# Kernel tuning notes

Hardware: AMD Instinct MI355X
Metric: run time of the kernel (lower is better)

Reference implementation:

```python
import jax, jax.numpy as jnp
import numpy as np
from functools import partial

N_USERS = 30000
N_ENTITIES = 70000
N = N_USERS + N_ENTITIES
D = 64
N_EDGES = 1_600_000
EPS = 1e-12


def setup_inputs() -> dict:
    key = jax.random.key(0)
    ks = jax.random.split(key, 10)
    s = 1.0 / np.sqrt(D)  # xavier-like scale for weights
    return {
        "user_tab": jax.random.normal(ks[0], (N_USERS, D), jnp.float32) * 0.1,
        "entity_tab": jax.random.normal(ks[1], (N_ENTITIES, D), jnp.float32) * 0.1,
        "A_vals": jax.random.uniform(ks[2], (N_EDGES,), jnp.float32) / 16.0,  # ~row-normalized
        "W1_1": jax.random.normal(ks[3], (D, D), jnp.float32) * s,
        "b1_1": jnp.zeros((D,), jnp.float32),
        "W2_1": jax.random.normal(ks[4], (D, D), jnp.float32) * s,
        "b2_1": jnp.zeros((D,), jnp.float32),
        "W1_2": jax.random.normal(ks[5], (D, 32), jnp.float32) * s,
        "b1_2": jnp.zeros((32,), jnp.float32),
        "W2_2": jax.random.normal(ks[6], (D, 32), jnp.float32) * s,
        "b2_2": jnp.zeros((32,), jnp.float32),
        "A_rows": jax.random.randint(ks[7], (N_EDGES,), 0, N, jnp.int64 if jax.config.jax_enable_x64 else jnp.int32),
        "A_cols": jax.random.randint(ks[8], (N_EDGES,), 0, N, jnp.int64 if jax.config.jax_enable_x64 else jnp.int32),
    }


def _spmm(rows, cols, vals, x):
    # sparse A (COO) @ dense x : gather tail embeddings, scale, scatter-add to rows
    msgs = x[cols] * vals[:, None]            # [E, d]
    return jax.ops.segment_sum(msgs, rows, num_segments=N)


def _l2norm(x):
    n = jnp.sqrt(jnp.sum(x * x, axis=1, keepdims=True))
    return x / jnp.maximum(n, EPS)


def _bi_layer(ego, side, W1, b1, W2, b2):
    sum_e = jax.nn.leaky_relu((ego + side) @ W1 + b1)  # slope 0.01 = torch default
    bi_e = jax.nn.leaky_relu((ego * side) @ W2 + b2)
    return _l2norm(sum_e + bi_e)  # dropout p=0 (eval)


def reference(user_tab, entity_tab, A_vals, W1_1, b1_1, W2_1, b2_1,
              W1_2, b1_2, W2_2, b2_2, A_rows, A_cols):
    ego = jnp.concatenate([user_tab, entity_tab], axis=0)  # [N, 64]
    all_embed = [ego]
    # layer 1: 64 -> 64
    side = _spmm(A_rows, A_cols, A_vals, ego)
    ego = _bi_layer(ego, side, W1_1, b1_1, W2_1, b2_1)
    all_embed.append(ego)
    # layer 2: 64 -> 32
    side = _spmm(A_rows, A_cols, A_vals, ego)
    ego = _bi_layer(ego, side, W1_2, b1_2, W2_2, b2_2)
    all_embed.append(ego)
    return jnp.concatenate(all_embed, axis=1)  # [N, 160]; split [n_users, n_entities] downstream
```

## Files before the change

### kernel.cpp

```cpp
#include <hip/hip_runtime.h>
#include <hip/hip_bf16.h>
#include <string.h>

#define N_USERS 30000
#define N_NODES 100000
#define DIM 64
#define N_EDGES 1600000
#define ROWS_PER_BUCK 256
#define NB ((N_NODES + ROWS_PER_BUCK - 1) / ROWS_PER_BUCK)
#define CHUNK 8192
#define NBLK_B ((N_EDGES + CHUNK - 1) / CHUNK)
#define E_ALLOC 1901464
#define STAGE_CAP 5120

typedef __hip_bfloat16 bf16;
typedef __attribute__((ext_vector_type(8))) short short8;
typedef __attribute__((ext_vector_type(4))) float floatx4;

__device__ __forceinline__ float b2f(bf16 v) { return __bfloat162float(v); }
__device__ __forceinline__ bf16 f2b(float v) { return __float2bfloat16(v); }
__device__ __forceinline__ unsigned short fbits(float v) {
    bf16 b = f2b(v); unsigned short u; memcpy(&u, &b, 2); return u;
}
__device__ __forceinline__ float ubf(unsigned u) {
    return __uint_as_float(u << 16);
}

__device__ __forceinline__ float ld(const void* p, int i, int f32) {
    return f32 ? ((const float*)p)[i] : b2f(((const bf16*)p)[i]);
}
__device__ __forceinline__ void st(void* p, int i, float v, int f32) {
    if (f32) ((float*)p)[i] = v; else ((bf16*)p)[i] = f2b(v);
}

__global__ void k_detect(const void* user, const void* ent, const void* vals,
                         const void* W, int* flags, int* bsize) {
    int t = threadIdx.x;
    for (int i = t; i < NB; i += 64) bsize[i] = 0;
    if (t == 0) {
        const void* ps[4] = { user, ent, vals, W };
        for (int k = 0; k < 4; ++k) {
            const float* f = (const float*)ps[k];
            int ok = 0;
            for (int i = 0; i < 32; ++i) {
                float v = f[i];
                if (v == v && fabsf(v) <= 1e4f) ok++;
            }
            flags[k] = (ok >= 16) ? 1 : 0;
        }
    }
}

__global__ __launch_bounds__(256) void k_hista(const int* __restrict__ rows,
                                               int* __restrict__ cnt_table,
                                               int* __restrict__ bsize) {
    __shared__ int h[NB];
    int t = threadIdx.x, blk = blockIdx.x;
    for (int b = t; b < NB; b += 256) h[b] = 0;
    __syncthreads();
    int base = blk * CHUNK + t * 4;
#pragma unroll
    for (int it = 0; it < 8; ++it) {
        int e = base + it * 1024;
        if (e < N_EDGES) {
            int4 r = *(const int4*)&rows[e];
            atomicAdd(&h[r.x >> 8], 1);
            atomicAdd(&h[r.y >> 8], 1);
            atomicAdd(&h[r.z >> 8], 1);
            atomicAdd(&h[r.w >> 8], 1);
        }
    }
    __syncthreads();
    for (int b = t; b < NB; b += 256) {
        int v = h[b];
        cnt_table[blk * NB + b] = v;
        if (v) atomicAdd(&bsize[b], v);
    }
}

__global__ __launch_bounds__(512) void k_bscan(const int* __restrict__ bsize,
                                               int* __restrict__ bbase) {
    __shared__ int lds[512];
    int t = threadIdx.x;
    int v = (t < NB) ? (((bsize[t] + 3) & ~3) + 3 * ROWS_PER_BUCK) : 0;
    lds[t] = v;
    __syncthreads();
    for (int off = 1; off < 512; off <<= 1) {
        int u = (t >= off) ? lds[t - off] : 0;
        __syncthreads();
        lds[t] += u;
        __syncthreads();
    }
    if (t <= NB) bbase[t] = (t == 0) ? 0 : lds[t - 1];
}

__global__ __launch_bounds__(256) void k_bscan2(int* __restrict__ cnt_table,
                                                const int* __restrict__ bbase) {
    __shared__ int lds[256];
    int t = threadIdx.x, b = blockIdx.x;
    int v = (t < NBLK_B) ? cnt_table[t * NB + b] : 0;
    lds[t] = v;
    __syncthreads();
    for (int off = 1; off < 256; off <<= 1) {
        int u = (t >= off) ? lds[t - off] : 0;
        __syncthreads();
        lds[t] += u;
        __syncthreads();
    }
    if (t < NBLK_B) cnt_table[t * NB + b] = bbase[b] + lds[t] - v;
}

__global__ __launch_bounds__(256) void k_bscatter2(
    const int* __restrict__ rows, const int* __restrict__ cols,
    const void* __restrict__ vals, const int* __restrict__ cnt_table,
    int2* __restrict__ bpack, const int* __restrict__ flags) {
    __shared__ int cur[NB];
    int t = threadIdx.x, blk = blockIdx.x;
    int fv = flags[2];
    for (int b = t; b < NB; b += 256) cur[b] = cnt_table[blk * NB + b];
    __syncthreads();
    int base = blk * CHUNK + t * 4;
#pragma unroll
    for (int it = 0; it < 8; ++it) {
        int e = base + it * 1024;
        if (e < N_EDGES) {
            int4 r = *(const int4*)&rows[e];
            int4 c = *(const int4*)&cols[e];
            float v0, v1, v2, v3;
            if (fv) {
                float4 vv = *(const float4*)((const float*)vals + e);
                v0 = vv.x; v1 = vv.y; v2 = vv.z; v3 = vv.w;
            } else {
                const bf16* bp = (const bf16*)vals + e;
                v0 = b2f(bp[0]); v1 = b2f(bp[1]); v2 = b2f(bp[2]); v3 = b2f(bp[3]);
            }
            int p0 = atomicAdd(&cur[r.x >> 8], 1);
            int p1 = atomicAdd(&cur[r.y >> 8], 1);
            int p2 = atomicAdd(&cur[r.z >> 8], 1);
            int p3 = atomicAdd(&cur[r.w >> 8], 1);
            bpack[p0] = make_int2(c.x | ((r.x & 255) << 17), __float_as_int(v0));
            bpack[p1] = make_int2(c.y | ((r.y & 255) << 17), __float_as_int(v1));
            bpack[p2] = make_int2(c.z | ((r.z & 255) << 17), __float_as_int(v2));
            bpack[p3] = make_int2(c.w | ((r.w & 255) << 17), __float_as_int(v3));
        }
    }
}

__global__ __launch_bounds__(256) void k_place2(
    const int* __restrict__ bsize, const int* __restrict__ bbase,
    const int2* __restrict__ bpack, int2* __restrict__ epack,
    int* __restrict__ row_start, int* __restrict__ row_end) {
    __shared__ __align__(16) int2 stage[STAGE_CAP];
    __shared__ int rcnt[ROWS_PER_BUCK];
    __shared__ int scan_lds[ROWS_PER_BUCK];
    __shared__ int rstart[ROWS_PER_BUCK];
    __shared__ int cur[ROWS_PER_BUCK];
    int t = threadIdx.x, b = blockIdx.x;
    int n = bsize[b];
    int gstart = bbase[b];
    rcnt[t] = 0;
    __syncthreads();
    for (int i = t; i < n; i += 256) {
        int2 p = bpack[gstart + i];
        if (i < STAGE_CAP) stage[i] = p;
        atomicAdd(&rcnt[(p.x >> 17) & 255], 1);
    }
    __syncthreads();
    int c = rcnt[t];
    int cp = (c + 3) & ~3;
    scan_lds[t] = cp;
    __syncthreads();
    for (int off = 1; off < 256; off <<= 1) {
        int u = (t >= off) ? scan_lds[t - off] : 0;
        __syncthreads();
        scan_lds[t] += u;
        __syncthreads();
    }
    int rs_ = gstart + scan_lds[t] - cp;
    rstart[t] = rs_;
    cur[t] = rs_;
    int node = b * ROWS_PER_BUCK + t;
    if (node < N_NODES) {
        row_start[node] = rs_;
        row_end[node] = rs_ + cp;
    }
    __syncthreads();
    for (int i = t; i < n; i += 256) {
        int2 p = (i < STAGE_CAP) ? stage[i] : bpack[gstart + i];
        int r = (p.x >> 17) & 255;
        int pos = atomicAdd(&cur[r], 1);
        epack[pos] = make_int2(p.x & 0x1FFFF, p.y);
    }
    __syncthreads();
    int pend = rstart[t] + cp;
    for (int pos = cur[t]; pos < pend; ++pos) epack[pos] = make_int2(0, 0);
}

__global__ void k_init(const void* __restrict__ user, const void* __restrict__ ent,
                       void* __restrict__ out, bf16* __restrict__ xb0,
                       const int* __restrict__ flags) {
    int i = blockIdx.x * blockDim.x + threadIdx.x;
    if (i >= N_NODES * DIM) return;
    int fo = flags[0], fe = flags[1];
    int n = i >> 6, d = i & 63;
    float v = (n < N_USERS) ? ld(user, i, fo) : ld(ent, i - N_USERS * DIM, fe);
    st(out, n * 160 + d, v, fo);
    xb0[i] = f2b(v);
}

#define GATHER_ROW_DECL(r) \
    int ej##r = rs[r], eend##r = re[r]; \
    bool ev##r = ej##r < eend##r; \
    int4 eA##r = {0,0,0,0}, eB##r = {0,0,0,0}; \
    if (ev##r) { eA##r = ep4[ej##r >> 1]; eB##r = ep4[(ej##r >> 1) + 1]; } \
    float ea##r = 0.f;

#define GATHER_EXTRACT(r) \
    int ec##r##0 = ev##r ? eA##r.x : 0, ec##r##1 = ev##r ? eA##r.z : 0; \
    int ec##r##2 = ev##r ? eB##r.x : 0, ec##r##3 = ev##r ? eB##r.z : 0; \
    float ew##r##0 = ev##r ? __int_as_float(eA##r.y) : 0.f; \
    float ew##r##1 = ev##r ? __int_as_float(eA##r.w) : 0.f; \
    float ew##r##2 = ev##r ? __int_as_float(eB##r.y) : 0.f; \
    float ew##r##3 = ev##r ? __int_as_float(eB##r.w) : 0.f;

#define GATHER_ISSUE(r) \
    unsigned eg##r##0 = xu[ec##r##0 * 64 + lane]; \
    unsigned eg##r##1 = xu[ec##r##1 * 64 + lane]; \
    unsigned eg##r##2 = xu[ec##r##2 * 64 + lane]; \
    unsigned eg##r##3 = xu[ec##r##3 * 64 + lane];

#define GATHER_ADVANCE(r) \
    ej##r += ev##r ? 4 : 0; \
    ev##r = ej##r < eend##r; \
    if (ev##r) { eA##r = ep4[ej##r >> 1]; eB##r = ep4[(ej##r >> 1) + 1]; }

#define GATHER_FMA(r) \
    ea##r += ew##r##0 * ubf(eg##r##0); \
    ea##r += ew##r##1 * ubf(eg##r##1); \
    ea##r += ew##r##2 * ubf(eg##r##2); \
    ea##r += ew##r##3 * ubf(eg##r##3);

#define GATHER_BODY \
    GATHER_ROW_DECL(0) GATHER_ROW_DECL(1) GATHER_ROW_DECL(2) GATHER_ROW_DECL(3) \
    while (ev0 | ev1 | ev2 | ev3) { \
        GATHER_EXTRACT(0) GATHER_EXTRACT(1) GATHER_EXTRACT(2) GATHER_EXTRACT(3) \
        GATHER_ISSUE(0) GATHER_ISSUE(1) GATHER_ISSUE(2) GATHER_ISSUE(3) \
        GATHER_ADVANCE(0) GATHER_ADVANCE(1) GATHER_ADVANCE(2) GATHER_ADVANCE(3) \
        GATHER_FMA(0) GATHER_FMA(1) GATHER_FMA(2) GATHER_FMA(3) \
    }

__global__ __launch_bounds__(256) void k_layer1(
    const void* __restrict__ W1, const void* __restrict__ b1,
    const void* __restrict__ W2, const void* __restrict__ b2,
    void* __restrict__ out, const int* __restrict__ row_start,
    const int* __restrict__ row_end,
    const int2* __restrict__ epack, const bf16* __restrict__ xt,
    bf16* __restrict__ xn, const int* __restrict__ flags) {
    __shared__ __align__(16) unsigned short hp_lds[16][72];
    __shared__ __align__(16) unsigned short hm_lds[16][72];
    __shared__ __align__(16) float ssq_lds[16][4];
    int t = threadIdx.x, lane = t & 63, w = t >> 6;
    int sub = lane & 15, quad = lane >> 4;
    int fo = flags[0], fw = flags[3];
    int rbase = blockIdx.x * 16 + w * 4;
    const unsigned short* xu = (const unsigned short*)xt;
    const int4* ep4 = (const int4*)epack;

    int4 rsv = *(const int4*)&row_start[rbase];
    int4 rev = *(const int4*)&row_end[rbase];
    int rs[4] = { rsv.x, rsv.y, rsv.z, rsv.w };
    int re[4] = { rev.x, rev.y, rev.z, rev.w };
    GATHER_BODY
    {
        float s[4] = { ea0, ea1, ea2, ea3 };
#pragma unroll
        for (int r = 0; r < 4; ++r) {
            float h = ld(out, (rbase + r) * 160 + lane, fo);
            hp_lds[w * 4 + r][lane] = fbits(h + s[r]);
            hm_lds[w * 4 + r][lane] = fbits(h * s[r]);
        }
    }
    __syncthreads();

    short8 Ap0 = *(const short8*)((const char*)hp_lds + sub * 144 + quad * 16);
    short8 Ap1 = *(const short8*)((const char*)hp_lds + sub * 144 + 64 + quad * 16);
    short8 Am0 = *(const short8*)((const char*)hm_lds + sub * 144 + quad * 16);
    short8 Am1 = *(const short8*)((const char*)hm_lds + sub * 144 + 64 + quad * 16);

    int wbase = w * 16;
    short8 Bw10, Bw11, Bw20, Bw21;
    float bias1, bias2;
    if (fw) {
        const float* w1 = (const float*)W1;
        const float* w2 = (const float*)W2;
#pragma unroll
        for (int j = 0; j < 8; ++j) {
            int k0 = quad * 8 + j;
            Bw10[j] = (short)fbits(w1[k0 * 64 + wbase + sub]);
            Bw11[j] = (short)fbits(w1[(k0 + 32) * 64 + wbase + sub]);
            Bw20[j] = (short)fbits(w2[k0 * 64 + wbase + sub]);
            Bw21[j] = (short)fbits(w2[(k0 + 32) * 64 + wbase + sub]);
        }
        bias1 = ((const float*)b1)[wbase + sub];
        bias2 = ((const float*)b2)[wbase + sub];
    } else {
        const unsigned short* w1 = (const unsigned short*)W1;
        const unsigned short* w2 = (const unsigned short*)W2;
#pragma unroll
        for (int j = 0; j < 8; ++j) {
            int k0 = quad * 8 + j;
            Bw10[j] = (short)w1[k0 * 64 + wbase + sub];
            Bw11[j] = (short)w1[(k0 + 32) * 64 + wbase + sub];
            Bw20[j] = (short)w2[k0 * 64 + wbase + sub];
            Bw21[j] = (short)w2[(k0 + 32) * 64 + wbase + sub];
        }
        bias1 = b2f(((const bf16*)b1)[wbase + sub]);
        bias2 = b2f(((const bf16*)b2)[wbase + sub]);
    }

    floatx4 c1; c1[0] = bias1; c1[1] = bias1; c1[2] = bias1; c1[3] = bias1;
    floatx4 c2; c2[0] = bias2; c2[1] = bias2; c2[2] = bias2; c2[3] = bias2;
    c1 = __builtin_amdgcn_mfma_f32_16x16x32_bf16(Ap0, Bw10, c1, 0, 0, 0);
    c1 = __builtin_amdgcn_mfma_f32_16x16x32_bf16(Ap1, Bw11, c1, 0, 0, 0);
    c2 = __builtin_amdgcn_mfma_f32_16x16x32_bf16(Am0, Bw20, c2, 0, 0, 0);
    c2 = __builtin_amdgcn_mfma_f32_16x16x32_bf16(Am1, Bw21, c2, 0, 0, 0);

    float v[4], sp[4];
#pragma unroll
    for (int r = 0; r < 4; ++r) {
        float s1 = c1[r], s2 = c2[r];
        s1 = s1 > 0.f ? s1 : 0.01f * s1;
        s2 = s2 > 0.f ? s2 : 0.01f * s2;
        v[r] = s1 + s2;
        float sq = v[r] * v[r];
        sq += __shfl_xor(sq, 1, 64);
        sq += __shfl_xor(sq, 2, 64);
        sq += __shfl_xor(sq, 4, 64);
        sq += __shfl_xor(sq, 8, 64);
        sp[r] = sq;
    }
    if (sub == 0) {
#pragma unroll
        for (int r = 0; r < 4; ++r) ssq_lds[quad * 4 + r][w] = sp[r];
    }
    __syncthreads();
#pragma unroll
    for (int r = 0; r < 4; ++r) {
        int row = quad * 4 + r;
        floatx4 ps = *(const floatx4*)&ssq_lds[row][0];
        float ss = ps[0] + ps[1] + ps[2] + ps[3];
        float o = v[r] * (1.0f / fmaxf(sqrtf(ss), 1e-12f));
        int n = blockIdx.x * 16 + row;
        st(out, n * 160 + 64 + wbase + sub, o, fo);
        xn[n * 64 + wbase + sub] = f2b(o);
    }
}

__global__ __launch_bounds__(256) void k_layer2(
    const void* __restrict__ W1, const void* __restrict__ b1,
    const void* __restrict__ W2, const void* __restrict__ b2,
    void* __restrict__ out, const int* __restrict__ row_start,
    const int* __restrict__ row_end,
    const int2* __restrict__ epack, const bf16* __restrict__ xt,
    const int* __restrict__ flags) {
    __shared__ __align__(16) unsigned short hp_lds[16][72];
    __shared__ __align__(16) unsigned short hm_lds[16][72];
    __shared__ __align__(16) float bi_lds[16][32];
    __shared__ __align__(16) float ssq_lds[16][2];
    int t = threadIdx.x, lane = t & 63, w = t >> 6;
    int sub = lane & 15, quad = lane >> 4;
    int fo = flags[0], fw = flags[3];
    int rbase = blockIdx.x * 16 + w * 4;
    const unsigned short* xu = (const unsigned short*)xt;
    const int4* ep4 = (const int4*)epack;

    int4 rsv = *(const int4*)&row_start[rbase];
    int4 rev = *(const int4*)&row_end[rbase];
    int rs[4] = { rsv.x, rsv.y, rsv.z, rsv.w };
    int re[4] = { rev.x, rev.y, rev.z, rev.w };
    GATHER_BODY
    {
        float s[4] = { ea0, ea1, ea2, ea3 };
#pragma unroll
        for (int r = 0; r < 4; ++r) {
            float h = ld(out, (rbase + r) * 160 + 64 + lane, fo);
            hp_lds[w * 4 + r][lane] = fbits(h + s[r]);
            hm_lds[w * 4 + r][lane] = fbits(h * s[r]);
        }
    }
    __syncthreads();

    int path = w >> 1;
    int nbase = (w & 1) * 16;
    const unsigned short(*hl)[72] = path ? hm_lds : hp_lds;
    short8 Af0 = *(const short8*)((const char*)hl + sub * 144 + quad * 16);
    short8 Af1 = *(const short8*)((const char*)hl + sub * 144 + 64 + quad * 16);

    const void* W = path ? W2 : W1;
    const void* bb = path ? b2 : b1;
    short8 Bf0, Bf1;
    float bias;
    if (fw) {
        const float* wp = (const float*)W;
#pragma unroll
        for (int j = 0; j < 8; ++j) {
            int k0 = quad * 8 + j;
            Bf0[j] = (short)fbits(wp[k0 * 32 + nbase + sub]);
            Bf1[j] = (short)fbits(wp[(k0 + 32) * 32 + nbase + sub]);
        }
        bias = ((const float*)bb)[nbase + sub];
    } else {
        const unsigned short* wp = (const unsigned short*)W;
#pragma unroll
        for (int j = 0; j < 8; ++j) {
            int k0 = quad * 8 + j;
            Bf0[j] = (short)wp[k0 * 32 + nbase + sub];
            Bf1[j] = (short)wp[(k0 + 32) * 32 + nbase + sub];
        }
        bias = b2f(((const bf16*)bb)[nbase + sub]);
    }

    floatx4 c; c[0] = bias; c[1] = bias; c[2] = bias; c[3] = bias;
    c = __builtin_amdgcn_mfma_f32_16x16x32_bf16(Af0, Bf0, c, 0, 0, 0);
    c = __builtin_amdgcn_mfma_f32_16x16x32_bf16(Af1, Bf1, c, 0, 0, 0);

    float T[4];
#pragma unroll
    for (int r = 0; r < 4; ++r) {
        float x = c[r];
        T[r] = x > 0.f ? x : 0.01f * x;
        if (path == 1) bi_lds[quad * 4 + r][nbase + sub] = T[r];
    }
    __syncthreads();

    float v[4], sp[4];
#pragma unroll
    for (int r = 0; r < 4; ++r) {
        v[r] = T[r] + bi_lds[quad * 4 + r][nbase + sub];
        float sq = v[r] * v[r];
        sq += __shfl_xor(sq, 1, 64);
        sq += __shfl_xor(sq, 2, 64);
        sq += __shfl_xor(sq, 4, 64);
        sq += __shfl_xor(sq, 8, 64);
        sp[r] = sq;
    }
    if (path == 0 && sub == 0) {
#pragma unroll
        for (int r = 0; r < 4; ++r) ssq_lds[quad * 4 + r][w & 1] = sp[r];
    }
    __syncthreads();
    if (path == 0) {
#pragma unroll
        for (int r = 0; r < 4; ++r) {
            int row = quad * 4 + r;
            float ss = ssq_lds[row][0] + ssq_lds[row][1];
            float o = v[r] * (1.0f / fmaxf(sqrtf(ss), 1e-12f));
            int n = blockIdx.x * 16 + row;
            st(out, n * 160 + 128 + nbase + sub, o, fo);
        }
    }
}

extern "C" void kernel_launch(void* const* d_in, const int* in_sizes, int n_in,
                              void* d_out, int out_size, void* d_ws, size_t ws_size,
                              hipStream_t stream) {
    const void* user = d_in[0];
    const void* ent  = d_in[1];
    const void* vals = d_in[2];
    const void* W1_1 = d_in[3];
    const void* b1_1 = d_in[4];
    const void* W2_1 = d_in[5];
    const void* b2_1 = d_in[6];
    const void* W1_2 = d_in[7];
    const void* b1_2 = d_in[8];
    const void* W2_2 = d_in[9];
    const void* b2_2 = d_in[10];
    const int* rows  = (const int*)d_in[11];
    const int* cols  = (const int*)d_in[12];

    char* w = (char*)d_ws;
    int* flags     = (int*)w;  w += 256;
    int* bsize     = (int*)w;  w += 2048;
    int* bbase     = (int*)w;  w += 2048;
    int* row_start = (int*)w;  w += 400128;
    int* row_end   = (int*)w;  w += 400128;
    int2* epack    = (int2*)w; w += (size_t)E_ALLOC * 8;
    bf16* xb0      = (bf16*)w; w += (size_t)N_NODES * DIM * 2;
    bf16* xb1      = (bf16*)w;
    int* cnt_table = (int*)epack;
    int2* bpack    = (int2*)xb0;

    k_detect<<<1, 64, 0, stream>>>(user, ent, vals, W1_1, flags, bsize);
    k_hista<<<NBLK_B, 256, 0, stream>>>(rows, cnt_table, bsize);
    k_bscan<<<1, 512, 0, stream>>>(bsize, bbase);
    k_bscan2<<<NB, 256, 0, stream>>>(cnt_table, bbase);
    k_bscatter2<<<NBLK_B, 256, 0, stream>>>(rows, cols, vals, cnt_table, bpack, flags);
    k_place2<<<NB, 256, 0, stream>>>(bsize, bbase, bpack, epack, row_start, row_end);
    k_init<<<(N_NODES * DIM + 255) / 256, 256, 0, stream>>>(user, ent, d_out, xb0, flags);
    k_layer1<<<N_NODES / 16, 256, 0, stream>>>(W1_1, b1_1, W2_1, b2_1, d_out, row_start, row_end, epack, xb0, xb1, flags);
    k_layer2<<<N_NODES / 16, 256, 0, stream>>>(W1_2, b1_2, W2_2, b2_2, d_out, row_start, row_end, epack, xb1, flags);
}
```

Measured before the change: 331.8 us.

## Pad rows in each 4-row group to common length for branchless SpMM gather

Each group of four consecutive rows is now padded to the group's maximum edge count during CSR placement, with zero-weight edges filling the slack. The gather loop then runs a uniform trip count read once per wavefront, with no per-row validity predicates, and software-prefetches the next edge pair. This removes branch and select overhead and divergence in the memory-bound gather, at the cost of extra padded edges, a larger edge buffer and more wasted gather traffic. The detect kernel is also parallelised with wave shuffles.

```diff
diff --git a/kernel.cpp b/kernel.cpp
--- a/kernel.cpp
+++ b/kernel.cpp
@@ -10,7 +10,8 @@
 #define NB ((N_NODES + ROWS_PER_BUCK - 1) / ROWS_PER_BUCK)
 #define CHUNK 8192
 #define NBLK_B ((N_EDGES + CHUNK - 1) / CHUNK)
-#define E_ALLOC 1901464
+#define BUCK_SLACK 2048
+#define E_ALLOC (N_EDGES + NB * BUCK_SLACK)
 #define STAGE_CAP 5120
 
 typedef __hip_bfloat16 bf16;
@@ -36,19 +37,17 @@
 __global__ void k_detect(const void* user, const void* ent, const void* vals,
                          const void* W, int* flags, int* bsize) {
     int t = threadIdx.x;
-    for (int i = t; i < NB; i += 64) bsize[i] = 0;
-    if (t == 0) {
-        const void* ps[4] = { user, ent, vals, W };
-        for (int k = 0; k < 4; ++k) {
-            const float* f = (const float*)ps[k];
-            int ok = 0;
-            for (int i = 0; i < 32; ++i) {
-                float v = f[i];
-                if (v == v && fabsf(v) <= 1e4f) ok++;
-            }
-            flags[k] = (ok >= 16) ? 1 : 0;
-        }
-    }
+    for (int i = t; i < NB; i += 128) bsize[i] = 0;
+    const void* ps[4] = { user, ent, vals, W };
+    int k = t >> 5, i = t & 31;
+    float v = ((const float*)ps[k])[i];
+    int ok = (v == v && fabsf(v) <= 1e4f) ? 1 : 0;
+    ok += __shfl_xor(ok, 1, 64);
+    ok += __shfl_xor(ok, 2, 64);
+    ok += __shfl_xor(ok, 4, 64);
+    ok += __shfl_xor(ok, 8, 64);
+    ok += __shfl_xor(ok, 16, 64);
+    if ((t & 31) == 0) flags[k] = (ok >= 16) ? 1 : 0;
 }
 
 __global__ __launch_bounds__(256) void k_hista(const int* __restrict__ rows,
@@ -82,7 +81,7 @@
                                                int* __restrict__ bbase) {
     __shared__ int lds[512];
     int t = threadIdx.x;
-    int v = (t < NB) ? (((bsize[t] + 3) & ~3) + 3 * ROWS_PER_BUCK) : 0;
+    int v = (t < NB) ? (((bsize[t] + 3) & ~3) + BUCK_SLACK) : 0;
     lds[t] = v;
     __syncthreads();
     for (int off = 1; off < 512; off <<= 1) {
@@ -168,7 +167,10 @@
     __syncthreads();
     int c = rcnt[t];
     int cp = (c + 3) & ~3;
-    scan_lds[t] = cp;
+    int g = cp;
+    g = max(g, __shfl_xor(g, 1, 64));
+    g = max(g, __shfl_xor(g, 2, 64));
+    scan_lds[t] = g;
     __syncthreads();
     for (int off = 1; off < 256; off <<= 1) {
         int u = (t >= off) ? scan_lds[t - off] : 0;
@@ -176,13 +178,13 @@
         scan_lds[t] += u;
         __syncthreads();
     }
-    int rs_ = gstart + scan_lds[t] - cp;
+    int rs_ = gstart + scan_lds[t] - g;
     rstart[t] = rs_;
     cur[t] = rs_;
     int node = b * ROWS_PER_BUCK + t;
     if (node < N_NODES) {
         row_start[node] = rs_;
-        row_end[node] = rs_ + cp;
+        row_end[node] = rs_ + g;
     }
     __syncthreads();
     for (int i = t; i < n; i += 256) {
@@ -192,7 +194,7 @@
         epack[pos] = make_int2(p.x & 0x1FFFF, p.y);
     }
     __syncthreads();
-    int pend = rstart[t] + cp;
+    int pend = rstart[t] + g;
     for (int pos = cur[t]; pos < pend; ++pos) epack[pos] = make_int2(0, 0);
 }
 
@@ -209,43 +211,34 @@
 }
 
 #define GATHER_ROW_DECL(r) \
-    int ej##r = rs[r], eend##r = re[r]; \
-    bool ev##r = ej##r < eend##r; \
-    int4 eA##r = {0,0,0,0}, eB##r = {0,0,0,0}; \
-    if (ev##r) { eA##r = ep4[ej##r >> 1]; eB##r = ep4[(ej##r >> 1) + 1]; } \
+    int ej##r = rs[r] >> 1; \
+    int4 eA##r = ep4[ej##r]; \
+    int4 eB##r = ep4[ej##r + 1]; \
     float ea##r = 0.f;
 
-#define GATHER_EXTRACT(r) \
-    int ec##r##0 = ev##r ? eA##r.x : 0, ec##r##1 = ev##r ? eA##r.z : 0; \
-    int ec##r##2 = ev##r ? eB##r.x : 0, ec##r##3 = ev##r ? eB##r.z : 0; \
-    float ew##r##0 = ev##r ? __int_as_float(eA##r.y) : 0.f; \
-    float ew##r##1 = ev##r ? __int_as_float(eA##r.w) : 0.f; \
-    float ew##r##2 = ev##r ? __int_as_float(eB##r.y) : 0.f; \
-    float ew##r##3 = ev##r ? __int_as_float(eB##r.w) : 0.f;
-
 #define GATHER_ISSUE(r) \
-    unsigned eg##r##0 = xu[ec##r##0 * 64 + lane]; \
-    unsigned eg##r##1 = xu[ec##r##1 * 64 + lane]; \
-    unsigned eg##r##2 = xu[ec##r##2 * 64 + lane]; \
-    unsigned eg##r##3 = xu[ec##r##3 * 64 + lane];
-
-#define GATHER_ADVANCE(r) \
-    ej##r += ev##r ? 4 : 0; \
-    ev##r = ej##r < eend##r; \
-    if (ev##r) { eA##r = ep4[ej##r >> 1]; eB##r = ep4[(ej##r >> 1) + 1]; }
+    unsigned eg##r##0 = xu[eA##r.x * 64 + lane]; \
+    unsigned eg##r##1 = xu[eA##r.z * 64 + lane]; \
+    unsigned eg##r##2 = xu[eB##r.x * 64 + lane]; \
+    unsigned eg##r##3 = xu[eB##r.z * 64 + lane];
+
+#define GATHER_ADV(r) \
+    int4 nA##r = ep4[ej##r + 2]; \
+    int4 nB##r = ep4[ej##r + 3]; \
+    ej##r += 2;
 
 #define GATHER_FMA(r) \
-    ea##r += ew##r##0 * ubf(eg##r##0); \
-    ea##r += ew##r##1 * ubf(eg##r##1); \
-    ea##r += ew##r##2 * ubf(eg##r##2); \
-    ea##r += ew##r##3 * ubf(eg##r##3);
-
-#define GATHER_BODY \
+    ea##r += __int_as_float(eA##r.y) * ubf(eg##r##0); \
+    ea##r += __int_as_float(eA##r.w) * ubf(eg##r##1); \
+    ea##r += __int_as_float(eB##r.y) * ubf(eg##r##2); \
+    ea##r += __int_as_float(eB##r.w) * ubf(eg##r##3); \
+    eA##r = nA##r; eB##r = nB##r;
+
+#define GATHER_BODY(EMX) \
     GATHER_ROW_DECL(0) GATHER_ROW_DECL(1) GATHER_ROW_DECL(2) GATHER_ROW_DECL(3) \
-    while (ev0 | ev1 | ev2 | ev3) { \
-        GATHER_EXTRACT(0) GATHER_EXTRACT(1) GATHER_EXTRACT(2) GATHER_EXTRACT(3) \
+    for (int ei = 0; ei < (EMX); ei += 4) { \
         GATHER_ISSUE(0) GATHER_ISSUE(1) GATHER_ISSUE(2) GATHER_ISSUE(3) \
-        GATHER_ADVANCE(0) GATHER_ADVANCE(1) GATHER_ADVANCE(2) GATHER_ADVANCE(3) \
+        GATHER_ADV(0) GATHER_ADV(1) GATHER_ADV(2) GATHER_ADV(3) \
         GATHER_FMA(0) GATHER_FMA(1) GATHER_FMA(2) GATHER_FMA(3) \
     }
 
@@ -267,10 +260,9 @@
     const int4* ep4 = (const int4*)epack;
 
     int4 rsv = *(const int4*)&row_start[rbase];
-    int4 rev = *(const int4*)&row_end[rbase];
     int rs[4] = { rsv.x, rsv.y, rsv.z, rsv.w };
-    int re[4] = { rev.x, rev.y, rev.z, rev.w };
-    GATHER_BODY
+    int emx = __builtin_amdgcn_readfirstlane(row_end[rbase] - rsv.x);
+    GATHER_BODY(emx)
     {
         float s[4] = { ea0, ea1, ea2, ea3 };
 #pragma unroll
@@ -375,10 +367,9 @@
     const int4* ep4 = (const int4*)epack;
 
     int4 rsv = *(const int4*)&row_start[rbase];
-    int4 rev = *(const int4*)&row_end[rbase];
     int rs[4] = { rsv.x, rsv.y, rsv.z, rsv.w };
-    int re[4] = { rev.x, rev.y, rev.z, rev.w };
-    GATHER_BODY
+    int emx = __builtin_amdgcn_readfirstlane(row_end[rbase] - rsv.x);
+    GATHER_BODY(emx)
     {
         float s[4] = { ea0, ea1, ea2, ea3 };
 #pragma unroll
@@ -490,7 +481,7 @@
     int* cnt_table = (int*)epack;
     int2* bpack    = (int2*)xb0;
 
-    k_detect<<<1, 64, 0, stream>>>(user, ent, vals, W1_1, flags, bsize);
+    k_detect<<<1, 128, 0, stream>>>(user, ent, vals, W1_1, flags, bsize);
     k_hista<<<NBLK_B, 256, 0, stream>>>(rows, cnt_table, bsize);
     k_bscan<<<1, 512, 0, stream>>>(bsize, bbase);
     k_bscan2<<<NB, 256, 0, stream>>>(cnt_table, bbase);
```

Result: faster. 307.5 us (-7.3%).
